# Optimization experiments

Hardware: AMD Instinct MI355X
Metric: run time of the kernel (lower is better)

Reference implementation:

```python
import jax, jax.numpy as jnp
import numpy as np

B = 8192
G, K, D = 8, 1024, 64  # num_codebooks, codebook_size, code_dim
INIT_SCALE = 0.1


def setup_inputs() -> dict:
    key = jax.random.key(0)
    kz, kc = jax.random.split(key)
    z = jax.random.normal(kz, (B, G * D), dtype=jnp.float32)
    codebook = jax.random.uniform(kc, (G, K, D), dtype=jnp.float32,
                                  minval=-INIT_SCALE, maxval=INIT_SCALE)
    return {"z": z, "codebook": codebook}


def reference(z, codebook):
    # Eval-mode forward of GroupedVectorQuantizer (no EMA buffer mutation).
    b = z.shape[0]
    g, k, d = codebook.shape
    zg = z.reshape(b, g, d)                       # [B,G,D]
    # squared L2 distance via ||z||^2 + ||c||^2 - 2 z.c (avoids [B,G,K,D] diff tensor)
    z2 = jnp.sum(zg * zg, axis=-1, keepdims=True)           # [B,G,1]
    c2 = jnp.sum(codebook * codebook, axis=-1)[None]        # [1,G,K]
    zc = jnp.einsum('bgd,gkd->bgk', zg, codebook)           # [B,G,K]
    dist = z2 + c2 - 2.0 * zc                               # [B,G,K]
    indices = jnp.argmin(dist, axis=-1)                     # [B,G] int32
    # gather nearest codes per group
    zq = codebook[jnp.arange(g)[None, :], indices]          # [B,G,D]
    commitment_loss = jnp.mean((zg - jax.lax.stop_gradient(zq)) ** 2)
    codebook_loss = jnp.zeros((), dtype=z.dtype)
    # straight-through estimator
    z_st = zg + jax.lax.stop_gradient(zq - zg)
    quantized_flat = z_st.reshape(b, g * d)
    # codebook usage entropy / perplexity (pooled over batch and groups, as in torch)
    usage = jnp.zeros((k,), dtype=jnp.float32).at[indices.reshape(-1)].add(1.0) / (b * g)
    entropy = -jnp.sum(usage * jnp.log(usage + 1e-10))
    perplexity = jnp.exp(entropy)
    return quantized_flat, indices, commitment_loss, codebook_loss, entropy, perplexity
```

## Files before the change

kernel.cpp:

```cpp
#include <hip/hip_runtime.h>
#include <hip/hip_bf16.h>
#include <math.h>

#define NB 8192
#define NG 8
#define NK 1024
#define ND 64
#define GD 512
#define MARGIN 2.5e-4f

typedef __attribute__((ext_vector_type(8))) short short8;
typedef __attribute__((ext_vector_type(4))) float f32x4;

#define WS_C2_OFF   0
#define WS_STG_OFF  32768
#define WS_HIST_OFF (32768 + 2097152 + 1048576)
#define WS_PART_OFF (WS_HIST_OFF + 4096)

typedef const __attribute__((address_space(1))) unsigned int glds_src_t;
typedef __attribute__((address_space(3))) unsigned int glds_dst_t;

__device__ inline void bsplit(float v, short& hs, short& ls) {
    __hip_bfloat16 h = __float2bfloat16(v);
    float hf = __bfloat162float(h);
    __hip_bfloat16 l = __float2bfloat16(v - hf);
    hs = *reinterpret_cast<short*>(&h);
    ls = *reinterpret_cast<short*>(&l);
}

__device__ inline float wredsum(float v) {
#pragma unroll
    for (int st = 1; st < 64; st <<= 1) v += __shfl_xor(v, st);
    return v;
}

__global__ __launch_bounds__(64) void vq_prep(const float* __restrict__ cb,
                                              float* __restrict__ ws) {
    const int gid = blockIdx.x * 64 + threadIdx.x;
    const int g  = gid >> 10, k = gid & 1023;
    const int it = k >> 6,   row = k & 63;
    const float* c = cb + (size_t)gid * ND;
    char* base = (char*)ws + WS_STG_OFF + (size_t)(g * 16 + it) * 16384 + row * 128;

    float a0 = 0.f, a1 = 0.f, a2 = 0.f, a3 = 0.f;
#pragma unroll
    for (int j = 0; j < 8; ++j) {
        const float4 v0 = reinterpret_cast<const float4*>(c)[2 * j];
        const float4 v1 = reinterpret_cast<const float4*>(c)[2 * j + 1];
        a0 = fmaf(v0.x, v0.x, a0); a1 = fmaf(v0.y, v0.y, a1);
        a2 = fmaf(v0.z, v0.z, a2); a3 = fmaf(v0.w, v0.w, a3);
        a0 = fmaf(v1.x, v1.x, a0); a1 = fmaf(v1.y, v1.y, a1);
        a2 = fmaf(v1.z, v1.z, a2); a3 = fmaf(v1.w, v1.w, a3);
        short h0, l0, h1, l1, h2, l2, h3, l3;
        short h4, l4, h5, l5, h6, l6, h7, l7;
        bsplit(v0.x, h0, l0); bsplit(v0.y, h1, l1);
        bsplit(v0.z, h2, l2); bsplit(v0.w, h3, l3);
        bsplit(v1.x, h4, l4); bsplit(v1.y, h5, l5);
        bsplit(v1.z, h6, l6); bsplit(v1.w, h7, l7);
        short8 hs, ls;
        hs[0] = h0; hs[1] = h1; hs[2] = h2; hs[3] = h3;
        hs[4] = h4; hs[5] = h5; hs[6] = h6; hs[7] = h7;
        ls[0] = l0; ls[1] = l1; ls[2] = l2; ls[3] = l3;
        ls[4] = l4; ls[5] = l5; ls[6] = l6; ls[7] = l7;
        const int off = (j ^ (row & 7)) << 4;
        *reinterpret_cast<short8*>(base + off)        = hs;
        *reinterpret_cast<short8*>(base + 8192 + off) = ls;
    }
    ((float*)((char*)ws + WS_C2_OFF))[gid] = (a0 + a1) + (a2 + a3);
    if (gid < NK) ((unsigned*)((char*)ws + WS_HIST_OFF))[gid] = 0u;
}

__global__ __launch_bounds__(256, 4) void vq_score(const float* __restrict__ z,
                                                   const float* __restrict__ cb,
                                                   float* __restrict__ out,
                                                   float* __restrict__ ws) {
    __shared__ __align__(16) char smem[2][16384];
    __shared__ int winfo[4][16];
    const int tid  = threadIdx.x;
    const int w    = tid >> 6;
    const int lane = tid & 63;
    const int lo   = lane & 15, hi = lane >> 4;
    const int g    = blockIdx.y;
    const int rbase = blockIdx.x * 64 + w * 16;

    const char*  stg = (const char*)ws + WS_STG_OFF + (size_t)g * 16 * 16384;
    const float* c2g = (const float*)((const char*)ws + WS_C2_OFF) + g * NK;

    short8 Ah[2], Al[2];
#pragma unroll
    for (int ks = 0; ks < 2; ++ks) {
        const float* zp = z + (size_t)(rbase + lo) * GD + g * ND + ks * 32 + hi * 8;
        float vv[8];
        *reinterpret_cast<float4*>(&vv[0]) = reinterpret_cast<const float4*>(zp)[0];
        *reinterpret_cast<float4*>(&vv[4]) = reinterpret_cast<const float4*>(zp)[1];
#pragma unroll
        for (int e = 0; e < 8; ++e) {
            short hs, ls;
            bsplit(vv[e], hs, ls);
            Ah[ks][e] = hs;
            Al[ks][e] = ls;
        }
    }

    float best[4], b2[4];
    int   bk[4], k2[4];
#pragma unroll
    for (int q = 0; q < 4; ++q) { best[q] = 3.0e38f; b2[q] = 3.0e38f; bk[q] = 0; k2[q] = 0; }

    const int rowoff = lo * 128;
    const int swz0 = ((hi ^ (lo & 7)) << 4);
    const int swz1 = (((4 + hi) ^ (lo & 7)) << 4);
    char* lds0 = &smem[0][0];

    const char* src = stg;
    auto STAGE = [&](const char* s, unsigned dOff) {
#pragma unroll
        for (int i = 0; i < 4; ++i) {
            const int so = w * 4096 + i * 1024 + lane * 16;
            __builtin_amdgcn_global_load_lds(
                (glds_src_t*)(const void*)(s + so),
                (glds_dst_t*)(void*)(lds0 + dOff + so), 16, 0, 0);
        }
    };

    STAGE(src, 0u);
    src += 16384;
    __syncthreads();

#pragma unroll 1
    for (int it = 0; it < 16; ++it) {
        const int kb = it * 64;
        float c2v[4];
#pragma unroll
        for (int n = 0; n < 4; ++n) c2v[n] = c2g[kb + n * 16 + lo];

        const unsigned cur = (unsigned)(it & 1) * 16384u;
        if (it < 15) { STAGE(src, cur ^ 16384u); src += 16384; }

        const char* bufc = lds0 + cur;
        f32x4 acc[4] = {{0.f,0.f,0.f,0.f},{0.f,0.f,0.f,0.f},{0.f,0.f,0.f,0.f},{0.f,0.f,0.f,0.f}};
#pragma unroll
        for (int ks = 0; ks < 2; ++ks) {
            short8 bh[4], bl[4];
#pragma unroll
            for (int n = 0; n < 4; ++n) {
                const int off = n * 2048 + rowoff + (ks ? swz1 : swz0);
                bh[n] = *reinterpret_cast<const short8*>(bufc + off);
                bl[n] = *reinterpret_cast<const short8*>(bufc + 8192 + off);
            }
#pragma unroll
            for (int n = 0; n < 4; ++n)
                acc[n] = __builtin_amdgcn_mfma_f32_16x16x32_bf16(
                    ks ? Ah[1] : Ah[0], bh[n], acc[n], 0, 0, 0);
#pragma unroll
            for (int n = 0; n < 4; ++n)
                acc[n] = __builtin_amdgcn_mfma_f32_16x16x32_bf16(
                    ks ? Ah[1] : Ah[0], bl[n], acc[n], 0, 0, 0);
#pragma unroll
            for (int n = 0; n < 4; ++n)
                acc[n] = __builtin_amdgcn_mfma_f32_16x16x32_bf16(
                    ks ? Al[1] : Al[0], bh[n], acc[n], 0, 0, 0);
        }

#pragma unroll
        for (int n = 0; n < 4; ++n) {
            const int kv = kb + n * 16 + lo;
#pragma unroll
            for (int q = 0; q < 4; ++q) {
                const float s = fmaf(-2.0f, acc[n][q], c2v[n]);
                const bool lt  = s < best[q];
                const bool lt2 = s < b2[q];
                b2[q]   = lt ? best[q] : (lt2 ? s : b2[q]);
                k2[q]   = lt ? bk[q]   : (lt2 ? kv : k2[q]);
                best[q] = lt ? s : best[q];
                bk[q]   = lt ? kv : bk[q];
            }
        }
        __syncthreads();
    }

#pragma unroll
    for (int q = 0; q < 4; ++q) {
        float pb = best[q], p2 = b2[q];
        int   kq = bk[q],   kq2 = k2[q];
#pragma unroll
        for (int st = 1; st < 16; st <<= 1) {
            const float ob  = __shfl_xor(pb, st);
            const int   obk = __shfl_xor(kq, st);
            const float ob2 = __shfl_xor(p2, st);
            const int   ok2 = __shfl_xor(kq2, st);
            const bool bet = (ob < pb) || (ob == pb && obk < kq);
            const float lb  = bet ? pb : ob;
            const int   lk  = bet ? kq : obk;
            const float wb2 = bet ? ob2 : p2;
            const int   wk2 = bet ? ok2 : kq2;
            const bool s2 = (lb < wb2) || (lb == wb2 && lk < wk2);
            p2  = s2 ? lb : wb2;
            kq2 = s2 ? lk : wk2;
            pb  = bet ? ob : pb;
            kq  = bet ? obk : kq;
        }
        if (lo == 0) {
            const int ridx = hi * 4 + q;
            const bool fl = (p2 - pb) <= MARGIN;
            winfo[w][ridx] = kq | (kq2 << 10) | (fl ? (1 << 20) : 0);
        }
    }
    asm volatile("s_waitcnt lgkmcnt(0)" ::: "memory");
    __builtin_amdgcn_sched_barrier(0);

    const float* cgrp = cb + (size_t)g * NK * ND;
    int* wif = &winfo[w][0];
    float esum = 0.f;
#pragma unroll 1
    for (int r = 0; r < 16; ++r) {
        const int info = wif[r];
        const int row  = rbase + r;
        const float zd = z[(size_t)row * GD + g * ND + lane];
        int win = info & 1023;

        if (info & (1 << 20)) {
            const int kalt = (info >> 10) & 1023;
            const float z2 = wredsum(zd * zd);
            const float c1 = cgrp[(size_t)win * ND + lane];
            const float d1 = (z2 + c2g[win]) - 2.0f * wredsum(zd * c1);
            const float c2 = cgrp[(size_t)kalt * ND + lane];
            const float d2 = (z2 + c2g[kalt]) - 2.0f * wredsum(zd * c2);
            if (d2 < d1 || (d2 == d1 && kalt < win)) win = kalt;
            if (lane == 0) wif[r] = win;
        }

        const float cw = cgrp[(size_t)win * ND + lane];
        out[(size_t)row * GD + g * ND + lane] = zd + (cw - zd);
        const float e = zd - cw;
        esum += e * e;
    }

    asm volatile("s_waitcnt lgkmcnt(0)" ::: "memory");
    __builtin_amdgcn_sched_barrier(0);
    if (lane < 16) {
        const int wv = wif[lane] & 1023;
        out[(size_t)NB * GD + (size_t)(rbase + lane) * NG + g] = (float)wv;
        atomicAdd((unsigned*)((char*)ws + WS_HIST_OFF) + wv, 1u);
    }

    esum = wredsum(esum);
    __shared__ float sh[4];
    if (lane == 0) sh[w] = esum;
    __syncthreads();
    if (tid == 0)
        ((float*)((char*)ws + WS_PART_OFF))[blockIdx.y * 128 + blockIdx.x] =
            (sh[0] + sh[1]) + (sh[2] + sh[3]);
}

__global__ __launch_bounds__(1024) void vq_final(const float* __restrict__ ws,
                                                 float* __restrict__ out) {
    const int t = threadIdx.x;
    __shared__ float se[1024];
    __shared__ float sc[1024];
    const unsigned cnt = ((const unsigned*)((const char*)ws + WS_HIST_OFF))[t];
    const float usage = (float)cnt * (1.0f / 65536.f);
    se[t] = -usage * logf(usage + 1e-10f);
    const float* part = (const float*)((const char*)ws + WS_PART_OFF);
    sc[t] = part[t];
    __syncthreads();
    for (int st = 512; st > 0; st >>= 1) {
        if (t < st) {
            se[t] += se[t + st];
            sc[t] += sc[t + st];
        }
        __syncthreads();
    }
    if (t == 0) {
        float* scal = out + (size_t)NB * GD + (size_t)NB * NG;
        scal[0] = sc[0] * (1.0f / ((float)NB * NG * ND));
        scal[1] = 0.0f;
        scal[2] = se[0];
        scal[3] = expf(se[0]);
    }
}

extern "C" void kernel_launch(void* const* d_in, const int* in_sizes, int n_in,
                              void* d_out, int out_size, void* d_ws, size_t ws_size,
                              hipStream_t stream) {
    const float* z  = (const float*)d_in[0];
    const float* cb = (const float*)d_in[1];
    float* out = (float*)d_out;
    float* ws  = (float*)d_ws;

    hipLaunchKernelGGL(vq_prep,  dim3(128),    dim3(64),   0, stream, cb, ws);
    hipLaunchKernelGGL(vq_score, dim3(128, 8), dim3(256),  0, stream, z, cb, out, ws);
    hipLaunchKernelGGL(vq_final, dim3(1),      dim3(1024), 0, stream, ws, out);
}
```

Baseline: 58.91 us.

## Pack scores with tile index into uint keys for branchless top-2 tracking

Adds a bias to the codebook norms so that every score is positive, which lets the float bits be compared as unsigned integers. The low 4 mantissa bits are replaced by the iteration index, and the per-lane top-2 is tracked with umin/umax per accumulator slot. This replaces the compare/select chains that carried separate index registers. The cost is more registers (32 packed values) and lost low mantissa precision, which the larger near-tie margin must absorb through the exact re-check path.

```diff
diff --git a/kernel.cpp b/kernel.cpp
--- a/kernel.cpp
+++ b/kernel.cpp
@@ -7,18 +7,23 @@
 #define NK 1024
 #define ND 64
 #define GD 512
-#define MARGIN 2.5e-4f
+#define MARGIN 4.0e-4f
+#define BIAS 16.0f
 
 typedef __attribute__((ext_vector_type(8))) short short8;
 typedef __attribute__((ext_vector_type(4))) float f32x4;
 
 #define WS_C2_OFF   0
-#define WS_STG_OFF  32768
-#define WS_HIST_OFF (32768 + 2097152 + 1048576)
+#define WS_C2B_OFF  32768
+#define WS_STG_OFF  65536
+#define WS_HIST_OFF (65536 + 2097152)
 #define WS_PART_OFF (WS_HIST_OFF + 4096)
 
 typedef const __attribute__((address_space(1))) unsigned int glds_src_t;
 typedef __attribute__((address_space(3))) unsigned int glds_dst_t;
+
+__device__ inline unsigned umin2(unsigned a, unsigned b) { return a < b ? a : b; }
+__device__ inline unsigned umax2(unsigned a, unsigned b) { return a > b ? a : b; }
 
 __device__ inline void bsplit(float v, short& hs, short& ls) {
     __hip_bfloat16 h = __float2bfloat16(v);
@@ -66,7 +71,9 @@
         *reinterpret_cast<short8*>(base + off)        = hs;
         *reinterpret_cast<short8*>(base + 8192 + off) = ls;
     }
-    ((float*)((char*)ws + WS_C2_OFF))[gid] = (a0 + a1) + (a2 + a3);
+    const float c2s = (a0 + a1) + (a2 + a3);
+    ((float*)((char*)ws + WS_C2_OFF))[gid]  = c2s;
+    ((float*)((char*)ws + WS_C2B_OFF))[gid] = c2s + BIAS;
     if (gid < NK) ((unsigned*)((char*)ws + WS_HIST_OFF))[gid] = 0u;
 }
 
@@ -83,8 +90,9 @@
     const int g    = blockIdx.y;
     const int rbase = blockIdx.x * 64 + w * 16;
 
-    const char*  stg = (const char*)ws + WS_STG_OFF + (size_t)g * 16 * 16384;
-    const float* c2g = (const float*)((const char*)ws + WS_C2_OFF) + g * NK;
+    const char*  stg  = (const char*)ws + WS_STG_OFF + (size_t)g * 16 * 16384;
+    const float* c2g  = (const float*)((const char*)ws + WS_C2_OFF) + g * NK;
+    const float* c2bg = (const float*)((const char*)ws + WS_C2B_OFF) + g * NK;
 
     short8 Ah[2], Al[2];
 #pragma unroll
@@ -102,10 +110,11 @@
         }
     }
 
-    float best[4], b2[4];
-    int   bk[4], k2[4];
-#pragma unroll
-    for (int q = 0; q < 4; ++q) { best[q] = 3.0e38f; b2[q] = 3.0e38f; bk[q] = 0; k2[q] = 0; }
+    unsigned bestp[4][4], b2p[4][4];
+#pragma unroll
+    for (int n = 0; n < 4; ++n)
+#pragma unroll
+        for (int q = 0; q < 4; ++q) { bestp[n][q] = 0xFFFFFFFFu; b2p[n][q] = 0xFFFFFFFFu; }
 
     const int rowoff = lo * 128;
     const int swz0 = ((hi ^ (lo & 7)) << 4);
@@ -132,7 +141,7 @@
         const int kb = it * 64;
         float c2v[4];
 #pragma unroll
-        for (int n = 0; n < 4; ++n) c2v[n] = c2g[kb + n * 16 + lo];
+        for (int n = 0; n < 4; ++n) c2v[n] = c2bg[kb + n * 16 + lo];
 
         const unsigned cur = (unsigned)(it & 1) * 16384u;
         if (it < 15) { STAGE(src, cur ^ 16384u); src += 16384; }
@@ -163,37 +172,47 @@
         }
 
 #pragma unroll
-        for (int n = 0; n < 4; ++n) {
-            const int kv = kb + n * 16 + lo;
+        for (int n = 0; n < 4; ++n)
 #pragma unroll
             for (int q = 0; q < 4; ++q) {
                 const float s = fmaf(-2.0f, acc[n][q], c2v[n]);
-                const bool lt  = s < best[q];
-                const bool lt2 = s < b2[q];
-                b2[q]   = lt ? best[q] : (lt2 ? s : b2[q]);
-                k2[q]   = lt ? bk[q]   : (lt2 ? kv : k2[q]);
-                best[q] = lt ? s : best[q];
-                bk[q]   = lt ? kv : bk[q];
+                const unsigned pk = (__float_as_uint(s) & 0xFFFFFFF0u) | (unsigned)it;
+                b2p[n][q]   = umin2(b2p[n][q], umax2(bestp[n][q], pk));
+                bestp[n][q] = umin2(bestp[n][q], pk);
             }
-        }
         __syncthreads();
     }
 
 #pragma unroll
     for (int q = 0; q < 4; ++q) {
-        float pb = best[q], p2 = b2[q];
-        int   kq = bk[q],   kq2 = k2[q];
+        unsigned pb = bestp[0][q], p2 = b2p[0][q];
+        int nb = 0, n2 = 0;
+#pragma unroll
+        for (int n = 1; n < 4; ++n) {
+            const unsigned cv  = bestp[n][q];
+            const unsigned cb2 = b2p[n][q];
+            const bool take = cv < pb;
+            const unsigned loser  = take ? pb : cv;
+            const int      nloser = take ? nb : n;
+            pb = take ? cv : pb;
+            nb = take ? n : nb;
+            if (loser < p2 || (loser == p2 && nloser < n2)) { p2 = loser; n2 = nloser; }
+            if (cb2 < p2 || (cb2 == p2 && n < n2))          { p2 = cb2;   n2 = n; }
+        }
+        int kq  = (int)(pb & 15u) * 64 + nb * 16 + lo;
+        int kq2 = (int)(p2 & 15u) * 64 + n2 * 16 + lo;
+
 #pragma unroll
         for (int st = 1; st < 16; st <<= 1) {
-            const float ob  = __shfl_xor(pb, st);
-            const int   obk = __shfl_xor(kq, st);
-            const float ob2 = __shfl_xor(p2, st);
-            const int   ok2 = __shfl_xor(kq2, st);
+            const unsigned ob  = (unsigned)__shfl_xor((int)pb, st);
+            const int      obk = __shfl_xor(kq, st);
+            const unsigned ob2 = (unsigned)__shfl_xor((int)p2, st);
+            const int      ok2 = __shfl_xor(kq2, st);
             const bool bet = (ob < pb) || (ob == pb && obk < kq);
-            const float lb  = bet ? pb : ob;
-            const int   lk  = bet ? kq : obk;
-            const float wb2 = bet ? ob2 : p2;
-            const int   wk2 = bet ? ok2 : kq2;
+            const unsigned lb  = bet ? pb : ob;
+            const int      lk  = bet ? kq : obk;
+            const unsigned wb2 = bet ? ob2 : p2;
+            const int      wk2 = bet ? ok2 : kq2;
             const bool s2 = (lb < wb2) || (lb == wb2 && lk < wk2);
             p2  = s2 ? lb : wb2;
             kq2 = s2 ? lk : wk2;
@@ -201,8 +220,10 @@
             kq  = bet ? obk : kq;
         }
         if (lo == 0) {
+            const float fpb = __uint_as_float(pb & 0xFFFFFFF0u);
+            const float fp2 = __uint_as_float(p2 & 0xFFFFFFF0u);
             const int ridx = hi * 4 + q;
-            const bool fl = (p2 - pb) <= MARGIN;
+            const bool fl = (fp2 - fpb) <= MARGIN;
             winfo[w][ridx] = kq | (kq2 << 10) | (fl ? (1 << 20) : 0);
         }
     }
```

Result: no change. 58.07 us (median of 3 runs) (-1.4%).
